# Kernel optimization log

Hardware: AMD Instinct MI355X
Metric: run time of the kernel (lower is better)

Reference implementation:

```python
import jax, jax.numpy as jnp
import numpy as np

EMBED_DIM = 512
NUM_HEADS = 8
HEAD_DIM = EMBED_DIM // NUM_HEADS


def setup_inputs() -> dict:
    key = jax.random.key(0)
    ks = jax.random.split(key, 9)
    d = EMBED_DIM
    s = 1.0 / np.sqrt(d)
    inp = {
        "x": jax.random.normal(ks[0], (2, 4096, d), dtype=jnp.float32),
        # torch nn.Linear weights are [out, in]; we store them the same way
        "Wq": jax.random.uniform(ks[1], (d, d), jnp.float32, -s, s),
        "bq": jax.random.uniform(ks[2], (d,), jnp.float32, -s, s),
        "Wk": jax.random.uniform(ks[3], (d, d), jnp.float32, -s, s),
        "bk": jax.random.uniform(ks[4], (d,), jnp.float32, -s, s),
        "Wv": jax.random.uniform(ks[5], (d, d), jnp.float32, -s, s),
        "bv": jax.random.uniform(ks[6], (d,), jnp.float32, -s, s),
        "Wo": jax.random.uniform(ks[7], (d, d), jnp.float32, -s, s),
        "bo": jax.random.uniform(ks[8], (d,), jnp.float32, -s, s),
    }
    return inp


def reference(x, Wq, bq, Wk, bk, Wv, bv, Wo, bo):
    B, S, D = x.shape
    H, Hd = NUM_HEADS, HEAD_DIM

    def proj(W, b):  # torch Linear: x @ W.T + b
        y = jnp.einsum("bsd,ed->bse", x, W) + b
        return y.reshape(B, S, H, Hd).transpose(0, 2, 1, 3)  # [B,H,S,Hd]

    Q = proj(Wq, bq)
    K = proj(Wk, bk)
    V = proj(Wv, bv)

    scale = 1.0 / jnp.sqrt(jnp.float32(Hd))
    scores = jnp.einsum("bhqd,bhkd->bhqk", Q, K) * scale  # [B,H,S,S]
    attn = jax.nn.softmax(scores, axis=-1)
    out = jnp.einsum("bhqk,bhkd->bhqd", attn, V)  # [B,H,S,Hd]
    out = out.transpose(0, 2, 1, 3).reshape(B, S, D)
    return jnp.einsum("bsd,ed->bse", out, Wo) + bo
```

## Files before the change

kernel.cpp:

```cpp
#include <hip/hip_runtime.h>


typedef unsigned short ushortT;
typedef __attribute__((ext_vector_type(8))) short short8;
typedef __attribute__((ext_vector_type(4))) float f32x4;
typedef __attribute__((ext_vector_type(16))) float f32x16;
typedef __attribute__((ext_vector_type(4))) unsigned int uint4v;
typedef __attribute__((ext_vector_type(2))) unsigned int uint2v;

__device__ __forceinline__ ushortT f2bf(float f) {
    unsigned int u = __builtin_bit_cast(unsigned int, f);
    u += 0x7FFFu + ((u >> 16) & 1u);
    return (ushortT)(u >> 16);
}

__device__ __forceinline__ unsigned int cvtpk(float lo, float hi) {
    unsigned int d;
    asm("v_cvt_pk_bf16_f32 %0, %1, %2" : "=v"(d) : "v"(lo), "v"(hi));
    return d;
}

__device__ __forceinline__ uint4v pk8(f32x4 a0, f32x4 a1) {
    uint4v r = { cvtpk(a0[0], a0[1]), cvtpk(a0[2], a0[3]),
                 cvtpk(a1[0], a1[1]), cvtpk(a1[2], a1[3]) };
    return r;
}

__device__ __forceinline__ void plswap(unsigned int &a, unsigned int &b) {
    uint2v r = __builtin_amdgcn_permlane32_swap(a, b, false, false);
    a = r[0]; b = r[1];
}

__device__ __forceinline__ void gload16(const ushortT* g, ushortT* l) {
    __builtin_amdgcn_global_load_lds(
        (const __attribute__((address_space(1))) void*)g,
        (__attribute__((address_space(3))) void*)l, 16, 0, 0);
}

#define ALDK 72

__global__ __launch_bounds__(256) void prep(
    const float* __restrict__ x,  const float* __restrict__ Wq,
    const float* __restrict__ Wk, const float* __restrict__ Wv,
    const float* __restrict__ Wo,
    ushortT* __restrict__ xb, ushortT* __restrict__ wb)
{
    const int bid = blockIdx.x, t = threadIdx.x;
    const float* src; ushortT* dst; size_t base;
    if (bid < 2048) { src = x; dst = xb; base = (size_t)bid * 2048; }
    else {
        int r = bid - 2048, wsel = r >> 7, rb = r & 127;
        src = (wsel == 0) ? Wq : (wsel == 1) ? Wk : (wsel == 2) ? Wv : Wo;
        dst = wb + (size_t)wsel * 262144;
        base = (size_t)rb * 2048;
    }
    const size_t off = base + (size_t)t * 8;
    f32x4 a0 = *(const f32x4*)(src + off);
    f32x4 a1 = *(const f32x4*)(src + off + 4);
    *(uint4v*)(dst + off) = pk8(a0, a1);
}

__global__ __launch_bounds__(256) void proj_qkv(
    const ushortT* __restrict__ xb, const ushortT* __restrict__ wb,
    const float* __restrict__ bq, const float* __restrict__ bk,
    const float* __restrict__ bv,
    ushortT* __restrict__ Qw, ushortT* __restrict__ Kw,
    ushortT* __restrict__ Vtw, float qscale)
{
    __shared__ __align__(16) ushortT As[2][128 * 32];
    __shared__ __align__(16) ushortT Bs[2][128 * 32];
    const int t = threadIdx.x;
    const int w = t >> 6, lane = t & 63;
    const int quad = lane >> 4, l15 = lane & 15;
    const int z = blockIdx.z;
    const int arow0 = blockIdx.x * 128;
    const int brow0 = blockIdx.y * 128;
    const int wm = (w >> 1) * 64, wn = (w & 1) * 64;

    const ushortT* Wz = wb + (size_t)z * 262144;
    const float* bias = (z == 0) ? bq : (z == 1) ? bk : bv;

    const int srow = lane >> 2;
    const int scol = (lane & 3) * 8;
    const size_t asrc = (size_t)(arow0 + w * 32 + srow) * 512 + scol;
    const size_t bsrc = (size_t)(brow0 + w * 32 + srow) * 512 + scol;

    f32x4 acc[4][4] = {};

    gload16(xb + asrc,        As[0] + (w * 2 + 0) * 512);
    gload16(xb + asrc + 8192, As[0] + (w * 2 + 1) * 512);
    gload16(Wz + bsrc,        Bs[0] + (w * 2 + 0) * 512);
    gload16(Wz + bsrc + 8192, Bs[0] + (w * 2 + 1) * 512);
    __syncthreads();

    int cur = 0;
    for (int k0 = 0; k0 < 512; k0 += 32) {
        if (k0 < 480) {
            const int nb = cur ^ 1, kn = k0 + 32;
            gload16(xb + asrc + kn,        As[nb] + (w * 2 + 0) * 512);
            gload16(xb + asrc + kn + 8192, As[nb] + (w * 2 + 1) * 512);
            gload16(Wz + bsrc + kn,        Bs[nb] + (w * 2 + 0) * 512);
            gload16(Wz + bsrc + kn + 8192, Bs[nb] + (w * 2 + 1) * 512);
        }

        short8 af[4], bfr[4];
#pragma unroll
        for (int i = 0; i < 4; i++)
            af[i] = *(const short8*)(As[cur] + (wm + i * 16 + l15) * 32 + quad * 8);
#pragma unroll
        for (int i = 0; i < 4; i++)
            bfr[i] = *(const short8*)(Bs[cur] + (wn + i * 16 + l15) * 32 + quad * 8);
#pragma unroll
        for (int mi = 0; mi < 4; mi++)
#pragma unroll
            for (int ni = 0; ni < 4; ni++)
                acc[mi][ni] = __builtin_amdgcn_mfma_f32_16x16x32_bf16(
                    af[mi], bfr[ni], acc[mi][ni], 0, 0, 0);

        __syncthreads();
        cur ^= 1;
    }

    if (z < 2) {
        ushortT* Y = (z == 0) ? Qw : Kw;
        const float sc = (z == 0) ? qscale : 1.0f;
#pragma unroll
        for (int ni = 0; ni < 4; ni++) {
            int col = brow0 + wn + ni * 16 + l15;
            float bv_ = bias[col];
#pragma unroll
            for (int mi = 0; mi < 4; mi++)
#pragma unroll
                for (int r = 0; r < 4; r++) {
                    int row = arow0 + wm + mi * 16 + quad * 4 + r;
                    Y[(size_t)row * 512 + col] = f2bf((acc[mi][ni][r] + bv_) * sc);
                }
        }
    } else {
        const int bidx = arow0 >> 12;
        const int s0 = (arow0 & 4095) + wm;
#pragma unroll
        for (int ni = 0; ni < 4; ni++) {
            int ch = brow0 + wn + ni * 16 + l15;
            float bv_ = bias[ch];
            ushortT* vrow = Vtw + (size_t)bidx * 2097152 + (size_t)ch * 4096;
#pragma unroll
            for (int mi = 0; mi < 4; mi++) {
                int s = s0 + mi * 16 + quad * 4;
                unsigned int u0 = cvtpk(acc[mi][ni][0] + bv_, acc[mi][ni][1] + bv_);
                unsigned int u1 = cvtpk(acc[mi][ni][2] + bv_, acc[mi][ni][3] + bv_);
                uint2v st2 = { u0, u1 };
                *(uint2v*)(vrow + s) = st2;
            }
        }
    }
}

__global__ __launch_bounds__(256) void gemm_out(
    const ushortT* __restrict__ X, const ushortT* __restrict__ Wob,
    const float* __restrict__ bias, float* __restrict__ Y)
{
    __shared__ __align__(16) ushortT As[2][128 * 32];
    __shared__ __align__(16) ushortT Bs[2][128 * 32];
    const int t = threadIdx.x;
    const int w = t >> 6, lane = t & 63;
    const int quad = lane >> 4, l15 = lane & 15;
    const int bm = blockIdx.x * 128, bn = blockIdx.y * 128;
    const int wm = (w >> 1) * 64, wn = (w & 1) * 64;

    const int srow = lane >> 2;
    const int scol = (lane & 3) * 8;
    const size_t asrc = (size_t)(bm + w * 32 + srow) * 512 + scol;
    const size_t bsrc = (size_t)(bn + w * 32 + srow) * 512 + scol;

    f32x4 acc[4][4] = {};

    gload16(X   + asrc,        As[0] + (w * 2 + 0) * 512);
    gload16(X   + asrc + 8192, As[0] + (w * 2 + 1) * 512);
    gload16(Wob + bsrc,        Bs[0] + (w * 2 + 0) * 512);
    gload16(Wob + bsrc + 8192, Bs[0] + (w * 2 + 1) * 512);
    __syncthreads();

    int cur = 0;
    for (int k0 = 0; k0 < 512; k0 += 32) {
        if (k0 < 480) {
            const int nb = cur ^ 1, kn = k0 + 32;
            gload16(X   + asrc + kn,        As[nb] + (w * 2 + 0) * 512);
            gload16(X   + asrc + kn + 8192, As[nb] + (w * 2 + 1) * 512);
            gload16(Wob + bsrc + kn,        Bs[nb] + (w * 2 + 0) * 512);
            gload16(Wob + bsrc + kn + 8192, Bs[nb] + (w * 2 + 1) * 512);
        }

        short8 af[4], bfr[4];
#pragma unroll
        for (int i = 0; i < 4; i++)
            af[i] = *(const short8*)(As[cur] + (wm + i * 16 + l15) * 32 + quad * 8);
#pragma unroll
        for (int i = 0; i < 4; i++)
            bfr[i] = *(const short8*)(Bs[cur] + (wn + i * 16 + l15) * 32 + quad * 8);
#pragma unroll
        for (int mi = 0; mi < 4; mi++)
#pragma unroll
            for (int ni = 0; ni < 4; ni++)
                acc[mi][ni] = __builtin_amdgcn_mfma_f32_16x16x32_bf16(
                    af[mi], bfr[ni], acc[mi][ni], 0, 0, 0);

        __syncthreads();
        cur ^= 1;
    }

#pragma unroll
    for (int ni = 0; ni < 4; ni++) {
        int col = bn + wn + ni * 16 + l15;
        float bv = bias[col];
#pragma unroll
        for (int mi = 0; mi < 4; mi++)
#pragma unroll
            for (int r = 0; r < 4; r++) {
                int row = bm + wm + mi * 16 + quad * 4 + r;
                Y[(size_t)row * 512 + col] = acc[mi][ni][r] + bv;
            }
    }
}

__device__ __forceinline__ void softmax_pack(const f32x16 &sacc, float &lp,
                                             uint4v &B0, uint4v &B1)
{
    float p[16];
#pragma unroll
    for (int r = 0; r < 16; r++) {
        p[r] = __builtin_amdgcn_exp2f(sacc[r]);
        lp += p[r];
    }
    unsigned int c00 = cvtpk(p[0],  p[1]),  c01 = cvtpk(p[2],  p[3]);
    unsigned int c10 = cvtpk(p[4],  p[5]),  c11 = cvtpk(p[6],  p[7]);
    unsigned int c20 = cvtpk(p[8],  p[9]),  c21 = cvtpk(p[10], p[11]);
    unsigned int c30 = cvtpk(p[12], p[13]), c31 = cvtpk(p[14], p[15]);
    plswap(c00, c10);
    plswap(c01, c11);
    plswap(c20, c30);
    plswap(c21, c31);
    B0 = uint4v{ c00, c01, c10, c11 };
    B1 = uint4v{ c20, c21, c30, c31 };
}

__global__ __launch_bounds__(512, 2) void attn(
    const ushortT* Q, const ushortT* __restrict__ K,
    const ushortT* __restrict__ Vt, ushortT* O)
{
    __shared__ __align__(16) ushortT SM[2][2][2][64 * ALDK];

    const int t = threadIdx.x;
    const int w = t >> 6, lane = t & 63;
    const int half = w >> 2, qw = w & 3;
    const int l31 = lane & 31, hh = lane >> 5;

    const int j = blockIdx.x + (blockIdx.y << 4);
    const int qt = (j >> 3) & 15;
    const int bh = ((j & 7) << 1) | (j >> 7);

    const int b = bh >> 3, h = bh & 7;
    const size_t qbase = (size_t)b * 4096 + qt * 256 + qw * 64;

    short8 qf[2][4];
#pragma unroll
    for (int qg = 0; qg < 2; qg++) {
        const ushortT* qp = Q + (qbase + qg * 32 + l31) * 512 + h * 64 + hh * 8;
#pragma unroll
        for (int dk = 0; dk < 4; dk++)
            qf[qg][dk] = *(const short8*)(qp + dk * 16);
    }

    f32x16 oacc[2][2] = {};
    float lpart[2] = {};

    const int kofs = half * 2048;
    const ushortT* Kbase = K + ((size_t)b * 4096 + kofs) * 512 + h * 64;
    const ushortT* Vbase = Vt + (size_t)b * 2097152 + (size_t)h * 64 * 4096 + kofs;

    const int th = t & 255;
    const int srow = th >> 3, scol = (th & 7) * 8;
    uint4v kg[2], vg[2];

#pragma unroll
    for (int i = 0; i < 2; i++) {
        kg[i] = *(const uint4v*)(Kbase + (size_t)(srow + 32 * i) * 512 + scol);
        vg[i] = *(const uint4v*)(Vbase + (size_t)(srow + 32 * i) * 4096 + scol);
    }
#pragma unroll
    for (int i = 0; i < 2; i++) {
        *(uint4v*)(SM[0][half][0] + (srow + 32 * i) * ALDK + scol) = kg[i];
        *(uint4v*)(SM[1][half][0] + (srow + 32 * i) * ALDK + scol) = vg[i];
    }
    __syncthreads();

    for (int kt = 0; kt < 32; kt++) {
        const int cur = kt & 1;

        if (kt < 31) {
            const int kb = (kt + 1) * 64;
#pragma unroll
            for (int i = 0; i < 2; i++) {
                kg[i] = *(const uint4v*)(Kbase + (size_t)(kb + srow + 32 * i) * 512 + scol);
                vg[i] = *(const uint4v*)(Vbase + (size_t)(srow + 32 * i) * 4096 + kb + scol);
            }
        }

        const ushortT* Kt  = SM[0][half][cur];
        const ushortT* Vtl = SM[1][half][cur];

#pragma unroll
        for (int st = 0; st < 2; st++) {
            short8 kf[4];
#pragma unroll
            for (int dk = 0; dk < 4; dk++)
                kf[dk] = *(const short8*)(Kt + (st * 32 + l31) * ALDK + dk * 16 + hh * 8);
            f32x16 s0 = {}, s1 = {};
#pragma unroll
            for (int dk = 0; dk < 4; dk++) {
                s0 = __builtin_amdgcn_mfma_f32_32x32x16_bf16(kf[dk], qf[0][dk], s0, 0, 0, 0);
                s1 = __builtin_amdgcn_mfma_f32_32x32x16_bf16(kf[dk], qf[1][dk], s1, 0, 0, 0);
            }

            uint4v B00, B01, B10, B11;
            softmax_pack(s0, lpart[0], B00, B01);
            softmax_pack(s1, lpart[1], B10, B11);
            short8 p00 = __builtin_bit_cast(short8, B00);
            short8 p01 = __builtin_bit_cast(short8, B01);
            short8 p10 = __builtin_bit_cast(short8, B10);
            short8 p11 = __builtin_bit_cast(short8, B11);

#pragma unroll
            for (int dt = 0; dt < 2; dt++) {
                short8 vf0 = *(const short8*)(Vtl + (dt * 32 + l31) * ALDK + st * 32 + hh * 8);
                short8 vf1 = *(const short8*)(Vtl + (dt * 32 + l31) * ALDK + st * 32 + 16 + hh * 8);
                oacc[0][dt] = __builtin_amdgcn_mfma_f32_32x32x16_bf16(vf0, p00, oacc[0][dt], 0, 0, 0);
                oacc[0][dt] = __builtin_amdgcn_mfma_f32_32x32x16_bf16(vf1, p01, oacc[0][dt], 0, 0, 0);
                oacc[1][dt] = __builtin_amdgcn_mfma_f32_32x32x16_bf16(vf0, p10, oacc[1][dt], 0, 0, 0);
                oacc[1][dt] = __builtin_amdgcn_mfma_f32_32x32x16_bf16(vf1, p11, oacc[1][dt], 0, 0, 0);
            }
        }

        if (kt < 31) {
            const int nb = cur ^ 1;
#pragma unroll
            for (int i = 0; i < 2; i++) {
                *(uint4v*)(SM[0][half][nb] + (srow + 32 * i) * ALDK + scol) = kg[i];
                *(uint4v*)(SM[1][half][nb] + (srow + 32 * i) * ALDK + scol) = vg[i];
            }
        }
        __syncthreads();
    }

    float* scratch = (float*)&SM[0][0][0][0];
    float* prow = scratch + (size_t)(qw * 64 + lane) * 68;

    if (half == 1) {
#pragma unroll
        for (int qg = 0; qg < 2; qg++)
#pragma unroll
            for (int dt = 0; dt < 2; dt++)
#pragma unroll
                for (int m = 0; m < 4; m++) {
                    f32x4 v4 = { oacc[qg][dt][4 * m + 0], oacc[qg][dt][4 * m + 1],
                                 oacc[qg][dt][4 * m + 2], oacc[qg][dt][4 * m + 3] };
                    *(f32x4*)(prow + qg * 32 + dt * 16 + m * 4) = v4;
                }
        prow[64] = lpart[0];
        prow[65] = lpart[1];
    }
    __syncthreads();

    if (half == 0) {
#pragma unroll
        for (int qg = 0; qg < 2; qg++) {
            float sum = lpart[qg] + prow[64 + qg];
            float l = sum + __shfl_xor(sum, 32);
            float rl = 1.0f / l;

            ushortT* orow = O + (qbase + qg * 32 + l31) * 512 + h * 64 + hh * 4;
#pragma unroll
            for (int dt = 0; dt < 2; dt++)
#pragma unroll
                for (int m = 0; m < 4; m++) {
                    f32x4 v4 = *(const f32x4*)(prow + qg * 32 + dt * 16 + m * 4);
                    unsigned int u0 = cvtpk((oacc[qg][dt][4 * m + 0] + v4[0]) * rl,
                                            (oacc[qg][dt][4 * m + 1] + v4[1]) * rl);
                    unsigned int u1 = cvtpk((oacc[qg][dt][4 * m + 2] + v4[2]) * rl,
                                            (oacc[qg][dt][4 * m + 3] + v4[3]) * rl);
                    uint2v st2 = { u0, u1 };
                    *(uint2v*)(orow + dt * 32 + m * 8) = st2;
                }
        }
    }
}

extern "C" void kernel_launch(void* const* d_in, const int* in_sizes, int n_in,
                              void* d_out, int out_size, void* d_ws, size_t ws_size,
                              hipStream_t stream)
{
    const float* x  = (const float*)d_in[0];
    const float* Wq = (const float*)d_in[1];
    const float* bq = (const float*)d_in[2];
    const float* Wk = (const float*)d_in[3];
    const float* bk = (const float*)d_in[4];
    const float* Wv = (const float*)d_in[5];
    const float* bv = (const float*)d_in[6];
    const float* Wo = (const float*)d_in[7];
    const float* bo = (const float*)d_in[8];

    ushortT* ws  = (ushortT*)d_ws;
    ushortT* Qw  = ws;
    ushortT* Kw  = ws + 4194304;
    ushortT* Vtw = ws + 8388608;
    ushortT* xb  = ws + 12582912;
    ushortT* wbf = ws + 16777216;

    const float qscale = 0.125f * 1.44269504089f;

    prep<<<dim3(2560), 256, 0, stream>>>(x, Wq, Wk, Wv, Wo, xb, wbf);
    proj_qkv<<<dim3(64, 4, 3), 256, 0, stream>>>(
        xb, wbf, bq, bk, bv, Qw, Kw, Vtw, qscale);
    attn<<<dim3(16, 16), 512, 0, stream>>>(Qw, Kw, Vtw, Qw);
    gemm_out<<<dim3(64, 4), 256, 0, stream>>>(Qw, wbf + 786432, bo, (float*)d_out);
}
```

Before: 195.8 us.

## Split attention key range across two blocks and merge with combine kernel

The attention kernel now splits the key sequence across a grid z-dimension of two, so each block processes 1024 keys per half instead of 2048, doubling the block count from 256 to 512 to better fill the GPU. Unnormalized fp32 partial outputs and row sums are written to workspace, and a new combine kernel adds the two partials, normalizes, and packs to bf16. Launch bounds are raised to 4 blocks per SM. It relies on softmax without max subtraction (as before) so partials add directly, but adds an extra kernel launch plus fp32 partial traffic, and the workspace layout is rearranged so the partials alias the no-longer-needed xb buffer.

```diff
diff --git a/kernel.cpp b/kernel.cpp
--- a/kernel.cpp
+++ b/kernel.cpp
@@ -244,9 +244,10 @@
     B1 = uint4v{ c20, c21, c30, c31 };
 }
 
-__global__ __launch_bounds__(512, 2) void attn(
-    const ushortT* Q, const ushortT* __restrict__ K,
-    const ushortT* __restrict__ Vt, ushortT* O)
+__global__ __launch_bounds__(512, 4) void attn(
+    const ushortT* __restrict__ Q, const ushortT* __restrict__ K,
+    const ushortT* __restrict__ Vt,
+    float* __restrict__ Op, float* __restrict__ ls)
 {
     __shared__ __align__(16) ushortT SM[2][2][2][64 * ALDK];
 
@@ -254,6 +255,7 @@
     const int w = t >> 6, lane = t & 63;
     const int half = w >> 2, qw = w & 3;
     const int l31 = lane & 31, hh = lane >> 5;
+    const int z = blockIdx.z;
 
     const int j = blockIdx.x + (blockIdx.y << 4);
     const int qt = (j >> 3) & 15;
@@ -274,7 +276,7 @@
     f32x16 oacc[2][2] = {};
     float lpart[2] = {};
 
-    const int kofs = half * 2048;
+    const int kofs = z * 2048 + half * 1024;
     const ushortT* Kbase = K + ((size_t)b * 4096 + kofs) * 512 + h * 64;
     const ushortT* Vbase = Vt + (size_t)b * 2097152 + (size_t)h * 64 * 4096 + kofs;
 
@@ -294,10 +296,10 @@
     }
     __syncthreads();
 
-    for (int kt = 0; kt < 32; kt++) {
+    for (int kt = 0; kt < 16; kt++) {
         const int cur = kt & 1;
 
-        if (kt < 31) {
+        if (kt < 15) {
             const int kb = (kt + 1) * 64;
 #pragma unroll
             for (int i = 0; i < 2; i++) {
@@ -341,7 +343,7 @@
             }
         }
 
-        if (kt < 31) {
+        if (kt < 15) {
             const int nb = cur ^ 1;
 #pragma unroll
             for (int i = 0; i < 2; i++) {
@@ -372,27 +374,52 @@
     __syncthreads();
 
     if (half == 0) {
+        float* Oz = Op + (size_t)z * 4194304;
 #pragma unroll
         for (int qg = 0; qg < 2; qg++) {
             float sum = lpart[qg] + prow[64 + qg];
             float l = sum + __shfl_xor(sum, 32);
-            float rl = 1.0f / l;
-
-            ushortT* orow = O + (qbase + qg * 32 + l31) * 512 + h * 64 + hh * 4;
+
+            const int srel = qt * 256 + qw * 64 + qg * 32 + l31;
+            if (hh == 0)
+                ls[(size_t)z * 65536 + (size_t)bh * 4096 + srel] = l;
+
+            float* orow = Oz + (qbase + qg * 32 + l31) * 512 + h * 64 + hh * 4;
 #pragma unroll
             for (int dt = 0; dt < 2; dt++)
 #pragma unroll
                 for (int m = 0; m < 4; m++) {
                     f32x4 v4 = *(const f32x4*)(prow + qg * 32 + dt * 16 + m * 4);
-                    unsigned int u0 = cvtpk((oacc[qg][dt][4 * m + 0] + v4[0]) * rl,
-                                            (oacc[qg][dt][4 * m + 1] + v4[1]) * rl);
-                    unsigned int u1 = cvtpk((oacc[qg][dt][4 * m + 2] + v4[2]) * rl,
-                                            (oacc[qg][dt][4 * m + 3] + v4[3]) * rl);
-                    uint2v st2 = { u0, u1 };
-                    *(uint2v*)(orow + dt * 32 + m * 8) = st2;
+                    f32x4 o4 = { oacc[qg][dt][4 * m + 0] + v4[0],
+                                 oacc[qg][dt][4 * m + 1] + v4[1],
+                                 oacc[qg][dt][4 * m + 2] + v4[2],
+                                 oacc[qg][dt][4 * m + 3] + v4[3] };
+                    *(f32x4*)(orow + dt * 32 + m * 8) = o4;
                 }
         }
     }
+}
+
+__global__ __launch_bounds__(256) void combine(
+    const float* __restrict__ Op, const float* __restrict__ ls,
+    ushortT* __restrict__ O)
+{
+    const size_t e = ((size_t)blockIdx.x * 256 + threadIdx.x) * 8;
+    const int row = (int)(e >> 9);
+    const int col = (int)(e & 511);
+    const int b = row >> 12, s = row & 4095, h = col >> 6;
+    const size_t li = (size_t)(b * 8 + h) * 4096 + s;
+
+    const float rl = 1.0f / (ls[li] + ls[65536 + li]);
+
+    f32x4 a0 = *(const f32x4*)(Op + e);
+    f32x4 a1 = *(const f32x4*)(Op + e + 4);
+    f32x4 b0 = *(const f32x4*)(Op + 4194304 + e);
+    f32x4 b1 = *(const f32x4*)(Op + 4194304 + e + 4);
+#pragma unroll
+    for (int i = 0; i < 4; i++) { a0[i] = (a0[i] + b0[i]) * rl;
+                                  a1[i] = (a1[i] + b1[i]) * rl; }
+    *(uint4v*)(O + e) = pk8(a0, a1);
 }
 
 extern "C" void kernel_launch(void* const* d_in, const int* in_sizes, int n_in,
@@ -413,14 +440,17 @@
     ushortT* Qw  = ws;
     ushortT* Kw  = ws + 4194304;
     ushortT* Vtw = ws + 8388608;
-    ushortT* xb  = ws + 12582912;
-    ushortT* wbf = ws + 16777216;
+    ushortT* wbf = ws + 12582912;
+    ushortT* xb  = ws + 13631488;
+    float*   fOp = (float*)(ws + 13631488);
+    float*   fls = (float*)(ws + 30408704);
 
     const float qscale = 0.125f * 1.44269504089f;
 
     prep<<<dim3(2560), 256, 0, stream>>>(x, Wq, Wk, Wv, Wo, xb, wbf);
     proj_qkv<<<dim3(64, 4, 3), 256, 0, stream>>>(
         xb, wbf, bq, bk, bv, Qw, Kw, Vtw, qscale);
-    attn<<<dim3(16, 16), 512, 0, stream>>>(Qw, Kw, Vtw, Qw);
+    attn<<<dim3(16, 16, 2), 512, 0, stream>>>(Qw, Kw, Vtw, fOp, fls);
+    combine<<<dim3(2048), 256, 0, stream>>>(fOp, fls, Qw);
     gemm_out<<<dim3(64, 4), 256, 0, stream>>>(Qw, wbf + 786432, bo, (float*)d_out);
 }
```

After: 371.1 us. +89.5%, slower.
